# Optimization experiments

Measured on AMD Instinct MI355X. Metric: run time of the kernel, lower is better.

The kernel has to match this reference:

```python
import jax, jax.numpy as jnp
import numpy as np

B = 1024       # n_nodes
C = 128        # num_features (multiplicity of 0e in irreps_in)
L = 16         # num_ell = dim of coupling irreps 0e+1o+2e+3o
E = 10         # num_elements
Q = 3          # num_equivariance for 1o output (2*lmax+1)
# path counts (last dim of U tensors) per correlation order nu=1,2,3
P_0e = (1, 4, 23)
P_1o = (1, 6, 37)


def setup_inputs() -> dict:
    key = jax.random.key(0)
    ks = jax.random.split(key, 16)
    x = jax.random.normal(ks[0], (B, C, L), dtype=jnp.float32)
    elem = jax.random.randint(ks[1], (B,), 0, E)
    y = jax.nn.one_hot(elem, E, dtype=jnp.float32)  # one-hot element types
    # U tensors are constant (buffer) CG-derived coupling tensors; random stand-ins
    # with the exact shapes produced by U_matrix_real.
    U1_0e = jax.random.normal(ks[2], (L, P_0e[0]), dtype=jnp.float32)
    U2_0e = jax.random.normal(ks[3], (L, L, P_0e[1]), dtype=jnp.float32)
    U3_0e = jax.random.normal(ks[4], (L, L, L, P_0e[2]), dtype=jnp.float32)
    U1_1o = jax.random.normal(ks[5], (Q, L, P_1o[0]), dtype=jnp.float32)
    U2_1o = jax.random.normal(ks[6], (Q, L, L, P_1o[1]), dtype=jnp.float32)
    U3_1o = jax.random.normal(ks[7], (Q, L, L, L, P_1o[2]), dtype=jnp.float32)
    # per-element weights, init randn/num_params as in the torch module
    W1_0e = jax.random.normal(ks[8], (E, P_0e[0], C), dtype=jnp.float32) / P_0e[0]
    W2_0e = jax.random.normal(ks[9], (E, P_0e[1], C), dtype=jnp.float32) / P_0e[1]
    W3_0e = jax.random.normal(ks[10], (E, P_0e[2], C), dtype=jnp.float32) / P_0e[2]
    W1_1o = jax.random.normal(ks[11], (Q and E, P_1o[0], C), dtype=jnp.float32) / P_1o[0]
    W1_1o = jax.random.normal(ks[11], (E, P_1o[0], C), dtype=jnp.float32) / P_1o[0]
    W2_1o = jax.random.normal(ks[12], (E, P_1o[1], C), dtype=jnp.float32) / P_1o[1]
    W3_1o = jax.random.normal(ks[13], (E, P_1o[2], C), dtype=jnp.float32) / P_1o[2]
    return dict(x=x, y=y,
                U1_0e=U1_0e, U2_0e=U2_0e, U3_0e=U3_0e,
                W1_0e=W1_0e, W2_0e=W2_0e, W3_0e=W3_0e,
                U1_1o=U1_1o, U2_1o=U2_1o, U3_1o=U3_1o,
                W1_1o=W1_1o, W2_1o=W2_1o, W3_1o=W3_1o)


def _contract_0e(x, y, U1, U2, U3, W1, W2, W3):
    # correlation order 3 chain for a scalar (0e) output irrep
    out = jnp.einsum('wxik,ekc,bci,be->bcwx', U3, W3, x, y)            # [B,C,L,L]
    c = jnp.einsum('wxk,ekc,be->bcwx', U2, W2, y) + out
    out = jnp.einsum('bcwi,bci->bcw', c, x)                            # [B,C,L]
    c = jnp.einsum('wk,ekc,be->bcw', U1, W1, y) + out
    out = jnp.einsum('bci,bci->bc', c, x)                              # [B,C]
    return out


def _contract_1o(x, y, U1, U2, U3, W1, W2, W3):
    # correlation order 3 chain for a vector (1o) output irrep; w = equivariance dim (3)
    out = jnp.einsum('wxvik,ekc,bci,be->bcwxv', U3, W3, x, y)          # [B,C,3,L,L]
    c = jnp.einsum('wxvk,ekc,be->bcwxv', U2, W2, y) + out
    out = jnp.einsum('bcwxi,bci->bcwx', c, x)                          # [B,C,3,L]
    c = jnp.einsum('wxk,ekc,be->bcwx', U1, W1, y) + out
    out = jnp.einsum('bcwi,bci->bcw', c, x)                            # [B,C,3]
    return out.reshape(out.shape[0], -1)                                # [B,3C]


def reference(x, y, U1_0e, U2_0e, U3_0e, W1_0e, W2_0e, W3_0e,
              U1_1o, U2_1o, U3_1o, W1_1o, W2_1o, W3_1o):
    out0 = _contract_0e(x, y, U1_0e, U2_0e, U3_0e, W1_0e, W2_0e, W3_0e)
    out1 = _contract_1o(x, y, U1_1o, U2_1o, U3_1o, W1_1o, W2_1o, W3_1o)
    return jnp.concatenate([out0, out1], axis=-1)                       # [B, 4C]
```

## Files before the change

### kernel.cpp

```cpp
#include <hip/hip_runtime.h>

namespace {
constexpr int NB = 1024, NC = 128, NL = 16, NE = 10, NOUT = 4 * NC;
constexpr int NTHREADS = 256;
constexpr int NSPLIT = 2;
constexpr int P3_0 = 23, P2_0 = 4, P3_1 = 37, P2_1 = 6;
constexpr int TRI_P = 1040, DUO_P = 160, CSTRIDE = 1224;
constexpr int U3ROWS = P3_0 + 3 * P3_1;
constexpr int U2ROWS = P2_0 + 3 * P2_1;
constexpr int SYM3_FLOATS = U3ROWS * TRI_P;
constexpr int SYM2_FLOATS = U2ROWS * DUO_P;
constexpr int SYM_TOTAL = SYM3_FLOATS + SYM2_FLOATS;
constexpr int OFF_CNT = 0;
constexpr int OFF_NID = 16;
constexpr int OFF_SYM3A = 10272;
constexpr int OFF_SYM2A = OFF_SYM3A + SYM3_FLOATS;
constexpr int OFF_UW = OFF_SYM2A + SYM2_FLOATS;
constexpr int UW_PER_C = 4 * 1216;
constexpr int UW_FLOATS = NE * NC * UW_PER_C;
constexpr int WS_FULL = OFF_UW + UW_FLOATS;
}

__device__ __forceinline__ bool tri_from_padded(int t, int& ri, int& rj, int& rm) {
    int pos = 0;
    for (int i = 0; i < 16; ++i)
        for (int j = i; j < 16; ++j) {
            const int L = 16 - j, PL = (L + 3) & ~3;
            if (t < pos + PL) { ri = i; rj = j; rm = j + (t - pos); return (t - pos) < L; }
            pos += PL;
        }
    return false;
}
__device__ __forceinline__ bool duo_from_padded(int t, int& ri, int& rj) {
    int pos = 0;
    for (int i = 0; i < 16; ++i) {
        const int L = 16 - i, PL = (L + 3) & ~3;
        if (t < pos + PL) { ri = i; rj = i + (t - pos); return (t - pos) < L; }
        pos += PL;
    }
    return false;
}

__device__ __forceinline__ void sym_body(int n,
    const float* __restrict__ U3_0e, const float* __restrict__ U3_1o,
    const float* __restrict__ U2_0e, const float* __restrict__ U2_1o,
    float* __restrict__ dst) {
    if (n < SYM3_FLOATS) {
        const int kk = n / TRI_P, t = n - kk * TRI_P;
        int pass, k, P; const float* U;
        if (kk < P3_0) { pass = 0; k = kk; P = P3_0; U = U3_0e; }
        else { const int r = kk - P3_0; pass = 1 + r / P3_1; k = r - (pass - 1) * P3_1;
               P = P3_1; U = U3_1o + (size_t)(pass - 1) * 4096 * P3_1; }
        int i, j, m; float s = 0.f;
        if (tri_from_padded(t, i, j, m)) {
            auto u3 = [&](int a, int b, int c) {
                return U[(size_t)(((a << 4) + b) * 16 + c) * P + k]; };
            s = u3(i, j, m);
            if (i == j && j == m) {}
            else if (i == j) s += u3(i, m, i) + u3(m, i, i);
            else if (j == m) s += u3(j, i, j) + u3(j, j, i);
            else s += u3(i, m, j) + u3(j, i, m) + u3(j, m, i) + u3(m, i, j) + u3(m, j, i);
        }
        dst[n] = s;
    } else if (n < SYM_TOTAL) {
        const int r = n - SYM3_FLOATS;
        const int kk = r / DUO_P, t = r - kk * DUO_P;
        int pass, k, P; const float* U;
        if (kk < P2_0) { pass = 0; k = kk; P = P2_0; U = U2_0e; }
        else { const int q = kk - P2_0; pass = 1 + q / P2_1; k = q - (pass - 1) * P2_1;
               P = P2_1; U = U2_1o + (size_t)(pass - 1) * 256 * P2_1; }
        int i, j; float s = 0.f;
        if (duo_from_padded(t, i, j)) {
            auto u2 = [&](int a, int b) { return U[(size_t)((a << 4) + b) * P + k]; };
            s = u2(i, j) + (i < j ? u2(j, i) : 0.f);
        }
        dst[n] = s;
    }
}

__global__ void prep_kernel(const float* __restrict__ y,
                            const float* __restrict__ U3_0e, const float* __restrict__ U3_1o,
                            const float* __restrict__ U2_0e, const float* __restrict__ U2_1o,
                            float* __restrict__ ws) {
    const int bid = blockIdx.x, tid = threadIdx.x;
    if (bid < NE) {
        __shared__ int s_scan[NTHREADS];
        const int e = bid;
        unsigned pat = 0;
#pragma unroll
        for (int q = 0; q < 4; ++q)
            if (y[(tid * 4 + q) * NE + e] > 0.5f) pat |= (1u << q);
        const int lc = __popc(pat);
        s_scan[tid] = lc;
        __syncthreads();
#pragma unroll
        for (int off = 1; off < NTHREADS; off <<= 1) {
            const int add = (tid >= off) ? s_scan[tid - off] : 0;
            __syncthreads();
            s_scan[tid] += add;
            __syncthreads();
        }
        int* cnt = (int*)ws + OFF_CNT;
        int* nid = (int*)ws + OFF_NID + e * NB;
        int pos = s_scan[tid] - lc;
#pragma unroll
        for (int q = 0; q < 4; ++q)
            if (pat & (1u << q)) nid[pos++] = tid * 4 + q;
        if (tid == 0) cnt[e] = s_scan[NTHREADS - 1];
    } else {
        const int n = (bid - NE) * NTHREADS + tid;
        sym_body(n, U3_0e, U3_1o, U2_0e, U2_1o, ws + OFF_SYM3A);
    }
}

template <int P3c, int P2c>
__device__ __forceinline__ void uw_core(const float* __restrict__ sym3p,
                                        const float* __restrict__ sym2p,
                                        const float* __restrict__ s_w3,
                                        const float* __restrict__ s_w2,
                                        float* __restrict__ dst, int tid)
{
#pragma unroll 1
    for (int idx = tid; idx < (TRI_P / 4) * 4; idx += NTHREADS) {
        const int t4 = idx >> 2, ch = idx & 3;
        float ax = 0.f, ay = 0.f, az = 0.f, aw = 0.f;
#pragma unroll 4
        for (int k = 0; k < P3c; ++k) {
            const float4 u = *reinterpret_cast<const float4*>(sym3p + (size_t)k * TRI_P + 4 * t4);
            const float wch = s_w3[4 * k + ch];
            ax = fmaf(u.x, wch, ax); ay = fmaf(u.y, wch, ay);
            az = fmaf(u.z, wch, az); aw = fmaf(u.w, wch, aw);
        }
        *reinterpret_cast<float4*>(dst + (size_t)ch * UW_PER_C + 4 * t4) =
            make_float4(ax, ay, az, aw);
    }
    if (tid < (DUO_P / 4) * 4) {
        const int t4 = tid >> 2, ch = tid & 3;
        float ax = 0.f, ay = 0.f, az = 0.f, aw = 0.f;
#pragma unroll
        for (int k = 0; k < P2c; ++k) {
            const float4 u = *reinterpret_cast<const float4*>(sym2p + (size_t)k * DUO_P + 4 * t4);
            const float wch = s_w2[4 * k + ch];
            ax = fmaf(u.x, wch, ax); ay = fmaf(u.y, wch, ay);
            az = fmaf(u.z, wch, az); aw = fmaf(u.w, wch, aw);
        }
        *reinterpret_cast<float4*>(dst + (size_t)ch * UW_PER_C + 1040 + 4 * t4) =
            make_float4(ax, ay, az, aw);
    }
}

__global__ void __launch_bounds__(NTHREADS, 4) uw_build(
    const float* __restrict__ U1_0e, const float* __restrict__ U1_1o,
    const float* __restrict__ W1_0e, const float* __restrict__ W2_0e,
    const float* __restrict__ W3_0e,
    const float* __restrict__ W1_1o, const float* __restrict__ W2_1o,
    const float* __restrict__ W3_1o,
    float* __restrict__ ws)
{
    __shared__ __align__(16) float s_w3[4 * P3_1];
    __shared__ __align__(16) float s_w2[4 * P2_1];
    const int tid = threadIdx.x, bid = blockIdx.x;
    const int pass = bid / (NE * (NC / 4));
    const int rest = bid % (NE * (NC / 4));
    const int e = rest / (NC / 4), cg = (rest % (NC / 4)) * 4;

    const int P3c = pass == 0 ? P3_0 : P3_1;
    const int P2c = pass == 0 ? P2_0 : P2_1;
    const int k3b = pass == 0 ? 0 : P3_0 + (pass - 1) * P3_1;
    const int k2b = pass == 0 ? 0 : P2_0 + (pass - 1) * P2_1;
    const float* W3e = (pass == 0 ? W3_0e + (size_t)e * P3_0 * NC
                                  : W3_1o + (size_t)e * P3_1 * NC) + cg;
    const float* W2e = (pass == 0 ? W2_0e + (size_t)e * P2_0 * NC
                                  : W2_1o + (size_t)e * P2_1 * NC) + cg;
    const float* W1e = (pass == 0 ? W1_0e : W1_1o) + e * NC + cg;
    const float* U1p = pass == 0 ? U1_0e : U1_1o + (pass - 1) * NL;
    const float* sym3p = ws + OFF_SYM3A + (size_t)k3b * TRI_P;
    const float* sym2p = ws + OFF_SYM2A + (size_t)k2b * DUO_P;
    float* dst = ws + OFF_UW + (size_t)(e * NC + cg) * UW_PER_C + pass * 1216;

    if (tid < P3c) {
        *reinterpret_cast<float4*>(&s_w3[4 * tid]) =
            *reinterpret_cast<const float4*>(W3e + tid * NC);
    } else if (tid >= 64 && tid < 64 + P2c) {
        const int k = tid - 64;
        *reinterpret_cast<float4*>(&s_w2[4 * k]) =
            *reinterpret_cast<const float4*>(W2e + k * NC);
    } else if (tid >= 128 && tid < 192) {
        const int t = tid - 128;
        dst[(size_t)(t >> 4) * UW_PER_C + 1200 + (t & 15)] = U1p[t & 15] * W1e[t >> 4];
    }
    __syncthreads();

    if (pass == 0) uw_core<P3_0, P2_0>(sym3p, sym2p, s_w3, s_w2, dst, tid);
    else           uw_core<P3_1, P2_1>(sym3p, sym2p, s_w3, s_w2, dst, tid);
}

__global__ void __launch_bounds__(NTHREADS, 4) node_kernel(
    const float* __restrict__ x, const float* __restrict__ ws,
    float* __restrict__ out) {
    __shared__ __align__(16) float s_lds[4 * CSTRIDE];
    __shared__ int s_nid[NB];
    const int tid = threadIdx.x, bid = blockIdx.x;
    const int pass = bid / (NE * (NC / 4));
    const int rest = bid % (NE * (NC / 4));
    const int e = rest / (NC / 4);
    const int cg = (rest % (NC / 4)) * 4;

    const int* cnt = (const int*)ws + OFF_CNT;
    const int* nid = (const int*)ws + OFF_NID + e * NB;
    const int nn = cnt[e];

    for (int i = tid; i < nn; i += NTHREADS) s_nid[i] = nid[i];

    const float* uwbase = ws + OFF_UW + (size_t)(e * NC + cg) * UW_PER_C;
#pragma unroll 1
    for (int idx = tid; idx < 1216; idx += NTHREADS) {
        const int chs = idx / 304, rr = idx - chs * 304;
        const float4 v = *reinterpret_cast<const float4*>(
            uwbase + (size_t)chs * UW_PER_C + pass * 1216 + 4 * rr);
        *reinterpret_cast<float4*>(&s_lds[chs * CSTRIDE + 4 * rr]) = v;
    }
    __syncthreads();

    const int w = tid >> 6;
    const int lane = tid & 63;
    const int cc = cg + w;
    const float* Tch = s_lds + w * CSTRIDE;
    const int col = pass == 0 ? cc : NC + 3 * cc + (pass - 1);

#pragma unroll 1
    for (int base = 0; base < nn; base += 64) {
        const int slot = base + lane;
        const bool val = slot < nn;
        const int b = s_nid[val ? slot : 0];
        const float* xp = x + ((size_t)b * NC + cc) * NL;
        float xr[NL];
#pragma unroll
        for (int v4 = 0; v4 < 4; ++v4)
            reinterpret_cast<float4*>(xr)[v4] = reinterpret_cast<const float4*>(xp)[v4];

        float acc = 0.f;
        int t3 = 0, t2 = 0;
#pragma unroll
        for (int i = 0; i < 16; ++i) {
            float gi = Tch[1200 + i];
            const int L2 = 16 - i, PL2 = (L2 + 3) & ~3;
            float s2r[16];
#pragma unroll
            for (int q4 = 0; q4 < PL2 / 4; ++q4)
                reinterpret_cast<float4*>(s2r)[q4] =
                    *reinterpret_cast<const float4*>(Tch + TRI_P + t2 + 4 * q4);
            t2 += PL2;
#pragma unroll
            for (int jo = 0; jo < 16 - i; ++jo) {
                const int j = i + jo;
                float wv = s2r[jo];
                const int Lr = 16 - j, PLr = (Lr + 3) & ~3;
#pragma unroll
                for (int q4 = 0; q4 < PLr / 4; ++q4) {
                    const float4 tv = *reinterpret_cast<const float4*>(Tch + t3 + 4 * q4);
                    wv = fmaf(tv.x, xr[(j + 4 * q4 + 0) & 15], wv);
                    wv = fmaf(tv.y, xr[(j + 4 * q4 + 1) & 15], wv);
                    wv = fmaf(tv.z, xr[(j + 4 * q4 + 2) & 15], wv);
                    wv = fmaf(tv.w, xr[(j + 4 * q4 + 3) & 15], wv);
                }
                t3 += PLr;
                gi = fmaf(wv, xr[j], gi);
            }
            acc = fmaf(gi, xr[i], acc);
        }
        if (val) out[(size_t)b * NOUT + col] = acc;
    }
}

template <int P3, int P2>
__device__ __forceinline__ void build_gather_f(const float* __restrict__ U3,
                                               const float* __restrict__ U2,
                                               const float* __restrict__ s_w3,
                                               const float* __restrict__ s_w2,
                                               float* __restrict__ lds, int tid) {
#pragma unroll 1
    for (int t = tid; t < TRI_P; t += NTHREADS) {
        int i, j, m; const bool v = tri_from_padded(t, i, j, m);
        float a0 = 0, a1 = 0, a2 = 0, a3 = 0;
        if (v) {
            int ng = 1, g1 = 0, g2 = 0, g3 = 0, g4 = 0, g5 = 0;
            const int g0 = ((i * 16 + j) * 16 + m);
            if (i == j && j == m) { ng = 1; }
            else if (i == j) { g1 = ((i * 16 + m) * 16 + i); g2 = ((m * 16 + i) * 16 + i); ng = 3; }
            else if (j == m) { g1 = ((j * 16 + i) * 16 + j); g2 = ((j * 16 + j) * 16 + i); ng = 3; }
            else { g1 = ((i * 16 + m) * 16 + j); g2 = ((j * 16 + i) * 16 + m);
                   g3 = ((j * 16 + m) * 16 + i); g4 = ((m * 16 + i) * 16 + j);
                   g5 = ((m * 16 + j) * 16 + i); ng = 6; }
#pragma unroll 1
            for (int k = 0; k < P3; ++k) {
                float u = U3[(size_t)g0 * P3 + k];
                if (ng > 1) u += U3[(size_t)g1 * P3 + k] + U3[(size_t)g2 * P3 + k];
                if (ng == 6) u += U3[(size_t)g3 * P3 + k] + U3[(size_t)g4 * P3 + k]
                                + U3[(size_t)g5 * P3 + k];
                const float4 wk = reinterpret_cast<const float4*>(s_w3)[k];
                a0 = fmaf(u, wk.x, a0); a1 = fmaf(u, wk.y, a1);
                a2 = fmaf(u, wk.z, a2); a3 = fmaf(u, wk.w, a3);
            }
        }
        lds[0 * CSTRIDE + t] = a0; lds[1 * CSTRIDE + t] = a1;
        lds[2 * CSTRIDE + t] = a2; lds[3 * CSTRIDE + t] = a3;
    }
    if (tid < DUO_P) {
        int i, j; const bool v = duo_from_padded(tid, i, j);
        float a0 = 0, a1 = 0, a2 = 0, a3 = 0;
        if (v) {
#pragma unroll 1
            for (int k = 0; k < P2; ++k) {
                float u = U2[(size_t)((i << 4) + j) * P2 + k];
                if (i < j) u += U2[(size_t)((j << 4) + i) * P2 + k];
                const float4 wk = reinterpret_cast<const float4*>(s_w2)[k];
                a0 = fmaf(u, wk.x, a0); a1 = fmaf(u, wk.y, a1);
                a2 = fmaf(u, wk.z, a2); a3 = fmaf(u, wk.w, a3);
            }
        }
        lds[0 * CSTRIDE + TRI_P + tid] = a0; lds[1 * CSTRIDE + TRI_P + tid] = a1;
        lds[2 * CSTRIDE + TRI_P + tid] = a2; lds[3 * CSTRIDE + TRI_P + tid] = a3;
    }
}

__global__ void __launch_bounds__(NTHREADS, 4) symcon_fallback(
    const float* __restrict__ x, const float* __restrict__ y,
    const float* __restrict__ U1_0e, const float* __restrict__ U2_0e,
    const float* __restrict__ U3_0e,
    const float* __restrict__ W1_0e, const float* __restrict__ W2_0e,
    const float* __restrict__ W3_0e,
    const float* __restrict__ U1_1o, const float* __restrict__ U2_1o,
    const float* __restrict__ U3_1o,
    const float* __restrict__ W1_1o, const float* __restrict__ W2_1o,
    const float* __restrict__ W3_1o,
    float* __restrict__ out)
{
    __shared__ __align__(16) float s_lds[4 * CSTRIDE];
    __shared__ __align__(16) float s_w3[4 * P3_1 + 4];
    __shared__ __align__(16) float s_w2[4 * P2_1];
    __shared__ int s_nid[NB];
    __shared__ int s_scan[NTHREADS];

    const int tid = threadIdx.x;
    const int bid = blockIdx.x;
    const int s   = bid & 1;
    const int e   = (bid >> 1) % NE;
    const int cg  = (bid / (2 * NE)) * 4;

    unsigned pat = 0;
#pragma unroll
    for (int q = 0; q < 4; ++q)
        if (y[(tid * 4 + q) * NE + e] > 0.5f) pat |= (1u << q);
    const int lc = __popc(pat);
    s_scan[tid] = lc;
    __syncthreads();
#pragma unroll
    for (int off = 1; off < NTHREADS; off <<= 1) {
        const int add = (tid >= off) ? s_scan[tid - off] : 0;
        __syncthreads();
        s_scan[tid] += add;
        __syncthreads();
    }
    const int nn = s_scan[NTHREADS - 1];
    {
        int pos = s_scan[tid] - lc;
#pragma unroll
        for (int q = 0; q < 4; ++q)
            if (pat & (1u << q)) s_nid[pos++] = tid * 4 + q;
    }
    __syncthreads();

    const int half = (nn + 1) >> 1;
    const int l0 = s * half, l1 = min(nn, l0 + half);
    const int L = l1 - l0;
    if (L <= 0) return;

    const int w    = tid >> 6;
    const int ch   = (tid >> 4) & 3;
    const int nsub = tid & 15;
    const int cc   = cg + ch;
    const int chunk = (L + 3) >> 2;
    const int wbase = l0 + w * chunk;
    const int wend  = min(l1, wbase + chunk);
    const int iters = (chunk + 15) >> 4;
    const float* Tch = s_lds + ch * CSTRIDE;

#pragma unroll 1
    for (int pass = 0; pass < 4; ++pass) {
        const float* U3r = pass == 0 ? U3_0e : U3_1o + (size_t)(pass - 1) * 4096 * P3_1;
        const float* U2r = pass == 0 ? U2_0e : U2_1o + (size_t)(pass - 1) * 256 * P2_1;
        const float* U1p = (pass == 0 ? U1_0e : U1_1o + (pass - 1) * NL);
        const float* W3e = (pass == 0 ? W3_0e + (size_t)e * P3_0 * NC
                                      : W3_1o + (size_t)e * P3_1 * NC) + cg;
        const float* W2e = (pass == 0 ? W2_0e + (size_t)e * P2_0 * NC
                                      : W2_1o + (size_t)e * P2_1 * NC) + cg;
        const float* W1e = (pass == 0 ? W1_0e : W1_1o) + e * NC + cg;
        const int P3c = pass == 0 ? P3_0 : P3_1;
        const int P2c = pass == 0 ? P2_0 : P2_1;
        const int col = pass == 0 ? cc : NC + 3 * cc + (pass - 1);

        if (tid < 4 * P3c) {
            s_w3[tid] = W3e[(tid >> 2) * NC + (tid & 3)];
        } else if (tid >= 152 && tid < 152 + 4 * P2c) {
            const int t = tid - 152;
            s_w2[t] = W2e[(t >> 2) * NC + (t & 3)];
        } else if (tid >= 192) {
            const int t = tid - 192;
            s_lds[(t >> 4) * CSTRIDE + 1200 + (t & 15)] = U1p[t & 15] * W1e[t >> 4];
        }
        __syncthreads();

        if (pass == 0) build_gather_f<P3_0, P2_0>(U3r, U2r, s_w3, s_w2, s_lds, tid);
        else           build_gather_f<P3_1, P2_1>(U3r, U2r, s_w3, s_w2, s_lds, tid);
        __syncthreads();

#pragma unroll 1
        for (int it = 0; it < iters; ++it) {
            const int slot = wbase + it * 16 + nsub;
            const bool val = slot < wend;
            const int b = s_nid[val ? slot : l0];
            const float* xp = x + ((size_t)b * NC + cc) * NL;
            float xr[NL];
#pragma unroll
            for (int v4 = 0; v4 < 4; ++v4)
                reinterpret_cast<float4*>(xr)[v4] = reinterpret_cast<const float4*>(xp)[v4];

            float acc = 0.f;
            int t3 = 0, t2 = 0;
#pragma unroll
            for (int i = 0; i < 16; ++i) {
                float gi = Tch[1200 + i];
                const int L2 = 16 - i, PL2 = (L2 + 3) & ~3;
                float s2r[16];
#pragma unroll
                for (int q4 = 0; q4 < PL2 / 4; ++q4)
                    reinterpret_cast<float4*>(s2r)[q4] =
                        *reinterpret_cast<const float4*>(Tch + TRI_P + t2 + 4 * q4);
                t2 += PL2;
#pragma unroll
                for (int jo = 0; jo < 16 - i; ++jo) {
                    const int j = i + jo;
                    float wv = s2r[jo];
                    const int Lr = 16 - j, PLr = (Lr + 3) & ~3;
#pragma unroll
                    for (int q4 = 0; q4 < PLr / 4; ++q4) {
                        const float4 tv = *reinterpret_cast<const float4*>(Tch + t3 + 4 * q4);
                        wv = fmaf(tv.x, xr[(j + 4 * q4 + 0) & 15], wv);
                        wv = fmaf(tv.y, xr[(j + 4 * q4 + 1) & 15], wv);
                        wv = fmaf(tv.z, xr[(j + 4 * q4 + 2) & 15], wv);
                        wv = fmaf(tv.w, xr[(j + 4 * q4 + 3) & 15], wv);
                    }
                    t3 += PLr;
                    gi = fmaf(wv, xr[j], gi);
                }
                acc = fmaf(gi, xr[i], acc);
            }
            if (val) out[(size_t)b * NOUT + col] = acc;
        }
        __syncthreads();
    }
}

extern "C" void kernel_launch(void* const* d_in, const int* in_sizes, int n_in,
                              void* d_out, int out_size, void* d_ws, size_t ws_size,
                              hipStream_t stream) {
    const float* x     = (const float*)d_in[0];
    const float* y     = (const float*)d_in[1];
    const float* U1_0e = (const float*)d_in[2];
    const float* U2_0e = (const float*)d_in[3];
    const float* U3_0e = (const float*)d_in[4];
    const float* W1_0e = (const float*)d_in[5];
    const float* W2_0e = (const float*)d_in[6];
    const float* W3_0e = (const float*)d_in[7];
    const float* U1_1o = (const float*)d_in[8];
    const float* U2_1o = (const float*)d_in[9];
    const float* U3_1o = (const float*)d_in[10];
    const float* W1_1o = (const float*)d_in[11];
    const float* W2_1o = (const float*)d_in[12];
    const float* W3_1o = (const float*)d_in[13];
    float* out = (float*)d_out;
    float* ws = (float*)d_ws;

    if (ws_size >= (size_t)WS_FULL * sizeof(float)) {
        const int symBlocks = (SYM_TOTAL + NTHREADS - 1) / NTHREADS;
        hipLaunchKernelGGL(prep_kernel, dim3(NE + symBlocks), dim3(NTHREADS), 0, stream,
                           y, U3_0e, U3_1o, U2_0e, U2_1o, ws);
        hipLaunchKernelGGL(uw_build, dim3(4 * NE * (NC / 4)), dim3(NTHREADS), 0, stream,
                           U1_0e, U1_1o, W1_0e, W2_0e, W3_0e, W1_1o, W2_1o, W3_1o, ws);
        hipLaunchKernelGGL(node_kernel, dim3(4 * NE * (NC / 4)), dim3(NTHREADS), 0, stream,
                           x, ws, out);
    } else {
        hipLaunchKernelGGL(symcon_fallback, dim3(NE * (NC / 4) * NSPLIT), dim3(NTHREADS), 0, stream,
                           x, y, U1_0e, U2_0e, U3_0e, W1_0e, W2_0e, W3_0e,
                           U1_1o, U2_1o, U3_1o, W1_1o, W2_1o, W3_1o, out);
    }
}
```

Baseline: 103.2 us.

## Fuse UW table build into node kernel, building per-block tables in LDS

Removes the separate uw_build kernel and its large global UW workspace. Each node_kernel block now computes its own U·W contraction table directly into shared memory from the symmetrized U tensors and per-element weights, instead of writing it to global memory and reading it back. This saves one launch and a global write/read round trip. In exchange each block does the table arithmetic inline before its node loop, and the float4 stores become scalar LDS stores.

```diff
diff --git a/kernel.cpp b/kernel.cpp
--- a/kernel.cpp
+++ b/kernel.cpp
@@ -15,10 +15,7 @@
 constexpr int OFF_NID = 16;
 constexpr int OFF_SYM3A = 10272;
 constexpr int OFF_SYM2A = OFF_SYM3A + SYM3_FLOATS;
-constexpr int OFF_UW = OFF_SYM2A + SYM2_FLOATS;
-constexpr int UW_PER_C = 4 * 1216;
-constexpr int UW_FLOATS = NE * NC * UW_PER_C;
-constexpr int WS_FULL = OFF_UW + UW_FLOATS;
+constexpr int WS_REQ = OFF_SYM2A + SYM2_FLOATS;
 }
 
 __device__ __forceinline__ bool tri_from_padded(int t, int& ri, int& rj, int& rm) {
@@ -114,14 +111,14 @@
 }
 
 template <int P3c, int P2c>
-__device__ __forceinline__ void uw_core(const float* __restrict__ sym3p,
-                                        const float* __restrict__ sym2p,
-                                        const float* __restrict__ s_w3,
-                                        const float* __restrict__ s_w2,
-                                        float* __restrict__ dst, int tid)
+__device__ __forceinline__ void build_lds(const float* __restrict__ sym3p,
+                                          const float* __restrict__ sym2p,
+                                          const float* __restrict__ s_w3,
+                                          const float* __restrict__ s_w2,
+                                          float* __restrict__ s_lds, int tid)
 {
 #pragma unroll 1
-    for (int idx = tid; idx < (TRI_P / 4) * 4; idx += NTHREADS) {
+    for (int idx = tid; idx < TRI_P; idx += NTHREADS) {
         const int t4 = idx >> 2, ch = idx & 3;
         float ax = 0.f, ay = 0.f, az = 0.f, aw = 0.f;
 #pragma unroll 4
@@ -131,10 +128,10 @@
             ax = fmaf(u.x, wch, ax); ay = fmaf(u.y, wch, ay);
             az = fmaf(u.z, wch, az); aw = fmaf(u.w, wch, aw);
         }
-        *reinterpret_cast<float4*>(dst + (size_t)ch * UW_PER_C + 4 * t4) =
-            make_float4(ax, ay, az, aw);
-    }
-    if (tid < (DUO_P / 4) * 4) {
+        float* d = s_lds + ch * CSTRIDE + 4 * t4;
+        d[0] = ax; d[1] = ay; d[2] = az; d[3] = aw;
+    }
+    if (tid < DUO_P) {
         const int t4 = tid >> 2, ch = tid & 3;
         float ax = 0.f, ay = 0.f, az = 0.f, aw = 0.f;
 #pragma unroll
@@ -144,25 +141,28 @@
             ax = fmaf(u.x, wch, ax); ay = fmaf(u.y, wch, ay);
             az = fmaf(u.z, wch, az); aw = fmaf(u.w, wch, aw);
         }
-        *reinterpret_cast<float4*>(dst + (size_t)ch * UW_PER_C + 1040 + 4 * t4) =
-            make_float4(ax, ay, az, aw);
-    }
-}
-
-__global__ void __launch_bounds__(NTHREADS, 4) uw_build(
+        float* d = s_lds + ch * CSTRIDE + TRI_P + 4 * t4;
+        d[0] = ax; d[1] = ay; d[2] = az; d[3] = aw;
+    }
+}
+
+__global__ void __launch_bounds__(NTHREADS, 4) node_kernel(
+    const float* __restrict__ x, const float* __restrict__ ws,
     const float* __restrict__ U1_0e, const float* __restrict__ U1_1o,
     const float* __restrict__ W1_0e, const float* __restrict__ W2_0e,
     const float* __restrict__ W3_0e,
     const float* __restrict__ W1_1o, const float* __restrict__ W2_1o,
     const float* __restrict__ W3_1o,
-    float* __restrict__ ws)
-{
+    float* __restrict__ out) {
+    __shared__ __align__(16) float s_lds[4 * CSTRIDE];
     __shared__ __align__(16) float s_w3[4 * P3_1];
     __shared__ __align__(16) float s_w2[4 * P2_1];
+    __shared__ int s_nid[NB];
     const int tid = threadIdx.x, bid = blockIdx.x;
     const int pass = bid / (NE * (NC / 4));
     const int rest = bid % (NE * (NC / 4));
-    const int e = rest / (NC / 4), cg = (rest % (NC / 4)) * 4;
+    const int e = rest / (NC / 4);
+    const int cg = (rest % (NC / 4)) * 4;
 
     const int P3c = pass == 0 ? P3_0 : P3_1;
     const int P2c = pass == 0 ? P2_0 : P2_1;
@@ -176,7 +176,11 @@
     const float* U1p = pass == 0 ? U1_0e : U1_1o + (pass - 1) * NL;
     const float* sym3p = ws + OFF_SYM3A + (size_t)k3b * TRI_P;
     const float* sym2p = ws + OFF_SYM2A + (size_t)k2b * DUO_P;
-    float* dst = ws + OFF_UW + (size_t)(e * NC + cg) * UW_PER_C + pass * 1216;
+
+    const int* cnt = (const int*)ws + OFF_CNT;
+    const int* nid = (const int*)ws + OFF_NID + e * NB;
+    const int nn = cnt[e];
+    for (int i = tid; i < nn; i += NTHREADS) s_nid[i] = nid[i];
 
     if (tid < P3c) {
         *reinterpret_cast<float4*>(&s_w3[4 * tid]) =
@@ -187,39 +191,12 @@
             *reinterpret_cast<const float4*>(W2e + k * NC);
     } else if (tid >= 128 && tid < 192) {
         const int t = tid - 128;
-        dst[(size_t)(t >> 4) * UW_PER_C + 1200 + (t & 15)] = U1p[t & 15] * W1e[t >> 4];
+        s_lds[(t >> 4) * CSTRIDE + 1200 + (t & 15)] = U1p[t & 15] * W1e[t >> 4];
     }
     __syncthreads();
 
-    if (pass == 0) uw_core<P3_0, P2_0>(sym3p, sym2p, s_w3, s_w2, dst, tid);
-    else           uw_core<P3_1, P2_1>(sym3p, sym2p, s_w3, s_w2, dst, tid);
-}
-
-__global__ void __launch_bounds__(NTHREADS, 4) node_kernel(
-    const float* __restrict__ x, const float* __restrict__ ws,
-    float* __restrict__ out) {
-    __shared__ __align__(16) float s_lds[4 * CSTRIDE];
-    __shared__ int s_nid[NB];
-    const int tid = threadIdx.x, bid = blockIdx.x;
-    const int pass = bid / (NE * (NC / 4));
-    const int rest = bid % (NE * (NC / 4));
-    const int e = rest / (NC / 4);
-    const int cg = (rest % (NC / 4)) * 4;
-
-    const int* cnt = (const int*)ws + OFF_CNT;
-    const int* nid = (const int*)ws + OFF_NID + e * NB;
-    const int nn = cnt[e];
-
-    for (int i = tid; i < nn; i += NTHREADS) s_nid[i] = nid[i];
-
-    const float* uwbase = ws + OFF_UW + (size_t)(e * NC + cg) * UW_PER_C;
-#pragma unroll 1
-    for (int idx = tid; idx < 1216; idx += NTHREADS) {
-        const int chs = idx / 304, rr = idx - chs * 304;
-        const float4 v = *reinterpret_cast<const float4*>(
-            uwbase + (size_t)chs * UW_PER_C + pass * 1216 + 4 * rr);
-        *reinterpret_cast<float4*>(&s_lds[chs * CSTRIDE + 4 * rr]) = v;
-    }
+    if (pass == 0) build_lds<P3_0, P2_0>(sym3p, sym2p, s_w3, s_w2, s_lds, tid);
+    else           build_lds<P3_1, P2_1>(sym3p, sym2p, s_w3, s_w2, s_lds, tid);
     __syncthreads();
 
     const int w = tid >> 6;
@@ -482,14 +459,13 @@
     float* out = (float*)d_out;
     float* ws = (float*)d_ws;
 
-    if (ws_size >= (size_t)WS_FULL * sizeof(float)) {
+    if (ws_size >= (size_t)WS_REQ * sizeof(float)) {
         const int symBlocks = (SYM_TOTAL + NTHREADS - 1) / NTHREADS;
         hipLaunchKernelGGL(prep_kernel, dim3(NE + symBlocks), dim3(NTHREADS), 0, stream,
                            y, U3_0e, U3_1o, U2_0e, U2_1o, ws);
-        hipLaunchKernelGGL(uw_build, dim3(4 * NE * (NC / 4)), dim3(NTHREADS), 0, stream,
-                           U1_0e, U1_1o, W1_0e, W2_0e, W3_0e, W1_1o, W2_1o, W3_1o, ws);
         hipLaunchKernelGGL(node_kernel, dim3(4 * NE * (NC / 4)), dim3(NTHREADS), 0, stream,
-                           x, ws, out);
+                           x, ws, U1_0e, U1_1o, W1_0e, W2_0e, W3_0e,
+                           W1_1o, W2_1o, W3_1o, out);
     } else {
         hipLaunchKernelGGL(symcon_fallback, dim3(NE * (NC / 4) * NSPLIT), dim3(NTHREADS), 0, stream,
                            x, y, U1_0e, U2_0e, U3_0e, W1_0e, W2_0e, W3_0e,
```

Measured after the change: 106.5 us. 1.03x slower.
